# Kernel optimization log

Measured on AMD Instinct MI355X. Metric: run time of the kernel, lower is better.

## Reference

```python
import jax, jax.numpy as jnp
import numpy as np

N = 50000      # nodes
E = 800000     # edges (before self-loops)
FIN = 512      # in_channels
HID = 64       # hid_units[i]
HEADS = 8      # n_heads[i]
OUT = 40       # out_channels
NEG_SLOPE = 0.2


def setup_inputs() -> dict:
    key = jax.random.key(0)
    ks = jax.random.split(key, 16)
    d = {
        "x": jax.random.normal(ks[0], (N, FIN), dtype=jnp.float32),
        "edge_index": jax.random.randint(ks[1], (2, E), 0, N, dtype=jnp.int64),
        # layer 1: FIN -> HEADS*HID
        "W1": jax.random.normal(ks[2], (FIN, HEADS * HID), dtype=jnp.float32) * 0.05,
        "att_src1": jax.random.normal(ks[3], (HEADS, HID), dtype=jnp.float32) * 0.1,
        "att_dst1": jax.random.normal(ks[4], (HEADS, HID), dtype=jnp.float32) * 0.1,
        "b1": jnp.zeros((HEADS * HID,), dtype=jnp.float32),
        # layer 2: HEADS*HID -> HEADS*HID
        "W2": jax.random.normal(ks[5], (HEADS * HID, HEADS * HID), dtype=jnp.float32) * 0.05,
        "att_src2": jax.random.normal(ks[6], (HEADS, HID), dtype=jnp.float32) * 0.1,
        "att_dst2": jax.random.normal(ks[7], (HEADS, HID), dtype=jnp.float32) * 0.1,
        "b2": jnp.zeros((HEADS * HID,), dtype=jnp.float32),
        # output layer: HEADS*HID -> OUT, 1 head, concat=False
        "W3": jax.random.normal(ks[8], (HEADS * HID, OUT), dtype=jnp.float32) * 0.05,
        "att_src3": jax.random.normal(ks[9], (1, OUT), dtype=jnp.float32) * 0.1,
        "att_dst3": jax.random.normal(ks[10], (1, OUT), dtype=jnp.float32) * 0.1,
        "b3": jnp.zeros((OUT,), dtype=jnp.float32),
    }
    return d


def gat_conv(x, src, dst, W, a_src, a_dst, b, heads, out_ch, concat):
    # x: [N, Fin]; src/dst: [E'] (self-loops included)
    h = (x @ W).reshape(N, heads, out_ch)              # [N, H, C]
    alpha_src = jnp.sum(h * a_src[None], axis=-1)      # [N, H]
    alpha_dst = jnp.sum(h * a_dst[None], axis=-1)      # [N, H]
    e = jax.nn.leaky_relu(alpha_src[src] + alpha_dst[dst], NEG_SLOPE)  # [E', H]
    # segment softmax over edges grouped by target node
    m = jax.ops.segment_max(e, dst, num_segments=N)    # [N, H]
    ex = jnp.exp(e - m[dst])
    denom = jax.ops.segment_sum(ex, dst, num_segments=N)
    alpha = ex / denom[dst]                            # [E', H]
    out = jax.ops.segment_sum(h[src] * alpha[:, :, None], dst, num_segments=N)  # [N, H, C]
    out = out.reshape(N, heads * out_ch) if concat else out.mean(axis=1)
    return out + b


def reference(x, edge_index, W1, att_src1, att_dst1, b1,
              W2, att_src2, att_dst2, b2,
              W3, att_src3, att_dst3, b3):
    loop = jnp.arange(N, dtype=edge_index.dtype)
    src = jnp.concatenate([edge_index[0], loop])  # add_self_loops=True (PyG default)
    dst = jnp.concatenate([edge_index[1], loop])
    h = gat_conv(x, src, dst, W1, att_src1, att_dst1, b1, HEADS, HID, True)
    h = jax.nn.elu(h)  # dropout p=0.0 / eval -> identity
    h = gat_conv(h, src, dst, W2, att_src2, att_dst2, b2, HEADS, HID, True)
    h = jax.nn.elu(h)
    h = gat_conv(h, src, dst, W3, att_src3, att_dst3, b3, 1, OUT, False)
    return jax.nn.log_softmax(h, axis=1)
```

## Files before the change

kernel.cpp:

```cpp
#include <hip/hip_runtime.h>
#include <math.h>

#define NNODES 50000
#define NEDGES 800000
#define FINCH 512
#define HIDC 64
#define NHEADS 8
#define OUTC 40
#define NSLOPE 0.2f
#define NSB ((NNODES + 255) / 256)

typedef unsigned short ushort;
typedef unsigned int uint;
typedef unsigned char uchar;
typedef __attribute__((ext_vector_type(8))) short bf16x8;
typedef __attribute__((ext_vector_type(4))) float f32x4;
typedef __attribute__((ext_vector_type(2))) float f32x2;

#if __has_builtin(__builtin_amdgcn_cvt_pk_f32_fp8) && __has_builtin(__builtin_amdgcn_cvt_pk_fp8_f32)
#define HAS_FP8 1
#else
#define HAS_FP8 0
#endif

static __device__ __forceinline__ float leaky(float e) { return e > 0.f ? e : NSLOPE * e; }

static __device__ __forceinline__ float bf2f(ushort u) {
    union { unsigned int i; float f; } c; c.i = ((unsigned int)u) << 16; return c.f;
}
static __device__ __forceinline__ ushort f2bf(float f) {
    union { float f; unsigned int i; } c; c.f = f;
    unsigned int r = c.i + 0x7FFF + ((c.i >> 16) & 1);
    return (ushort)(r >> 16);
}
static __device__ __forceinline__ uint fkey(float f) {
    uint u = __float_as_uint(f);
    return (u & 0x80000000u) ? ~u : (u | 0x80000000u);
}
static __device__ __forceinline__ float fdec(uint k) {
    return __uint_as_float((k & 0x80000000u) ? (k & 0x7fffffffu) : ~k);
}

static __device__ __forceinline__ void gload16(const ushort* g, ushort* l) {
    __builtin_amdgcn_global_load_lds((const __attribute__((address_space(1))) void*)g,
                                     (__attribute__((address_space(3))) void*)l, 16, 0, 0);
}

__global__ __launch_bounds__(64) void k_detect(const int* __restrict__ ei, int* __restrict__ flag,
                                               uint* __restrict__ keys) {
    int lane = threadIdx.x;
    if (lane < 17) keys[lane] = fkey(-3.0e38f);
    int v = ei[2 * lane + 1];
    unsigned long long b = __ballot(v != 0);
    if (lane == 0) *flag = (b == 0ULL) ? 1 : 0;
}

static __device__ __forceinline__ int load_idx(const int* ei, int wide, int pos) {
    int v = wide ? ei[2 * (long long)pos] : ei[pos];
    v = v < 0 ? 0 : (v >= NNODES ? NNODES - 1 : v);
    return v;
}

__global__ void k_init_deg(int* __restrict__ deg) {
    int i = blockIdx.x * blockDim.x + threadIdx.x;
    if (i < NNODES) deg[i] = 1;
}

__global__ void k_count(const int* __restrict__ ei, const int* __restrict__ flag, int* __restrict__ deg) {
    int e = blockIdx.x * blockDim.x + threadIdx.x;
    if (e < NEDGES) {
        int d = load_idx(ei, *flag, NEDGES + e);
        atomicAdd(&deg[d], 1);
    }
}

__global__ __launch_bounds__(256) void k_bsum(const int* __restrict__ deg, int* __restrict__ bsum) {
    int i = blockIdx.x * 256 + threadIdx.x;
    int v = (i < NNODES) ? deg[i] : 0;
#pragma unroll
    for (int m = 32; m > 0; m >>= 1) v += __shfl_xor(v, m);
    __shared__ int ws[4];
    int wid = threadIdx.x >> 6, lane = threadIdx.x & 63;
    if (lane == 0) ws[wid] = v;
    __syncthreads();
    if (threadIdx.x == 0) bsum[blockIdx.x] = ws[0] + ws[1] + ws[2] + ws[3];
}

__global__ __launch_bounds__(64) void k_bscan(const int* __restrict__ bsum, int* __restrict__ bofs,
                                              int* __restrict__ offs) {
    const int lane = threadIdx.x;
    const int CH = (NSB + 63) / 64;
    int lo = lane * CH, hi = min(lo + CH, NSB);
    int s = 0;
    for (int i = lo; i < hi; i++) s += bsum[i];
    int x = s;
#pragma unroll
    for (int st = 1; st < 64; st <<= 1) { int v = __shfl_up(x, st); if (lane >= st) x += v; }
    int run = x - s;
    for (int i = lo; i < hi; i++) { bofs[i] = run; run += bsum[i]; }
    if (lane == 63) offs[NNODES] = run;
}

__global__ __launch_bounds__(256) void k_scan_final(const int* __restrict__ deg, const int* __restrict__ bofs,
                                                    int* __restrict__ offs, int* __restrict__ cur) {
    int b = blockIdx.x;
    int i = b * 256 + threadIdx.x;
    int v = (i < NNODES) ? deg[i] : 0;
    int lane = threadIdx.x & 63, wid = threadIdx.x >> 6;
    int x = v;
#pragma unroll
    for (int st = 1; st < 64; st <<= 1) { int t = __shfl_up(x, st); if (lane >= st) x += t; }
    __shared__ int ws[4];
    if (lane == 63) ws[wid] = x;
    __syncthreads();
    int wofs = 0;
#pragma unroll
    for (int w = 0; w < 4; w++) if (w < wid) wofs += ws[w];
    int excl = bofs[b] + wofs + x - v;
    if (i < NNODES) { offs[i] = excl; cur[i] = excl; }
}

__global__ void k_fill(const int* __restrict__ ei, const int* __restrict__ flag,
                       int* __restrict__ cur, int* __restrict__ csr) {
    int e = blockIdx.x * blockDim.x + threadIdx.x;
    if (e < NEDGES + NNODES) {
        int s, d;
        if (e < NEDGES) {
            int w = *flag;
            s = load_idx(ei, w, e);
            d = load_idx(ei, w, NEDGES + e);
        } else {
            s = e - NEDGES; d = s;
        }
        int pos = atomicAdd(&cur[d], 1);
        csr[pos] = s;
    }
}

template <int NH>
__global__ __launch_bounds__(256) void k_msrc(const float* __restrict__ src, uint* __restrict__ keys, int n) {
    float m = -3.0e38f;
    for (int i = blockIdx.x * 256 + threadIdx.x; i < n; i += gridDim.x * 256)
        m = fmaxf(m, src[i]);
    __shared__ float red[256];
    red[threadIdx.x] = m;
    __syncthreads();
    for (int st = 128; st >= NH; st >>= 1) {
        if (threadIdx.x < st) red[threadIdx.x] = fmaxf(red[threadIdx.x], red[threadIdx.x + st]);
        __syncthreads();
    }
    if (threadIdx.x < NH) atomicMax(&keys[threadIdx.x], fkey(red[threadIdx.x]));
}

__global__ void k_f2bf(const float* __restrict__ in, ushort* __restrict__ out, int n4) {
    int i = blockIdx.x * blockDim.x + threadIdx.x;
    if (i < n4) {
        float4 v = ((const float4*)in)[i];
        ushort4 o = make_ushort4(f2bf(v.x), f2bf(v.y), f2bf(v.z), f2bf(v.w));
        ((ushort4*)out)[i] = o;
    }
}

__global__ __launch_bounds__(256) void k_transpose(const float* __restrict__ W, ushort* __restrict__ Wt) {
    __shared__ float tile[32][33];
    int bx = blockIdx.x, by = blockIdx.y;
    int tx = threadIdx.x & 31, ty = threadIdx.x >> 5;
#pragma unroll
    for (int i = 0; i < 4; i++)
        tile[ty + i * 8][tx] = W[(size_t)(by * 32 + ty + i * 8) * 512 + bx * 32 + tx];
    __syncthreads();
#pragma unroll
    for (int i = 0; i < 4; i++)
        Wt[(size_t)(bx * 32 + ty + i * 8) * 512 + by * 32 + tx] = f2bf(tile[tx][ty + i * 8]);
}

__global__ __launch_bounds__(256) void k_transpose3(const float* __restrict__ W3, ushort* __restrict__ Wt3) {
    int idx = blockIdx.x * 256 + threadIdx.x;
    int c = idx >> 9, k = idx & 511;
    Wt3[idx] = (c < OUTC) ? f2bf(W3[(size_t)k * OUTC + c]) : 0;
}

template <int CMODE>
__global__ __launch_bounds__(512) void mfma_gemm2(const ushort* __restrict__ A, const ushort* __restrict__ Bt,
                                                  void* __restrict__ Cv,
                                                  const float* __restrict__ att_s, const float* __restrict__ att_d,
                                                  float* __restrict__ asrc, float* __restrict__ adst, int M) {
    __shared__ ushort Abuf[2][128 * 32];
    __shared__ ushort Bbuf[2][128 * 32];
    const int nwg = gridDim.x;
    const int q = nwg >> 3, r = nwg & 7;
    const int orig = blockIdx.x;
    const int xcd = orig & 7, ii = orig >> 3;
    const int wgid = (xcd < r ? xcd * (q + 1) : r * (q + 1) + (xcd - r) * q) + ii;
    const int row0 = (wgid >> 2) * 128, col0 = (wgid & 3) * 128;

    const int t = threadIdx.x;
    const int wid = t >> 6, lane = t & 63;
    const int wr = wid >> 1, wc = wid & 1;
    const int l15 = lane & 15, l4 = lane >> 4;
    const int arow = t >> 2, kb = t & 3;
    const int swz = (arow >> 1) & 3;
    const int ra = min(row0 + arow, M - 1);
    const ushort* gA = A + (size_t)ra * 512 + ((kb ^ swz) << 3);
    const ushort* gB = Bt + (size_t)(col0 + arow) * 512 + ((kb ^ swz) << 3);
    f32x4 acc[2][4] = {};

    gload16(gA, &Abuf[0][wid * 512]);
    gload16(gB, &Bbuf[0][wid * 512]);
    __syncthreads();
    int cur = 0;
    for (int k0 = 0; k0 < 512; k0 += 32) {
        if (k0 + 32 < 512) {
            gload16(gA + k0 + 32, &Abuf[cur ^ 1][wid * 512]);
            gload16(gB + k0 + 32, &Bbuf[cur ^ 1][wid * 512]);
        }
        bf16x8 af[2], bfr[4];
#pragma unroll
        for (int mr = 0; mr < 2; mr++) {
            int rr = wr * 32 + mr * 16 + l15;
            af[mr] = *(const bf16x8*)&Abuf[cur][rr * 32 + ((l4 ^ ((rr >> 1) & 3)) << 3)];
        }
#pragma unroll
        for (int nr = 0; nr < 4; nr++) {
            int cc = wc * 64 + nr * 16 + l15;
            bfr[nr] = *(const bf16x8*)&Bbuf[cur][cc * 32 + ((l4 ^ ((cc >> 1) & 3)) << 3)];
        }
#pragma unroll
        for (int mr = 0; mr < 2; mr++)
#pragma unroll
            for (int nr = 0; nr < 4; nr++)
                acc[mr][nr] = __builtin_amdgcn_mfma_f32_16x16x32_bf16(af[mr], bfr[nr], acc[mr][nr], 0, 0, 0);
        __syncthreads();
        cur ^= 1;
    }
#pragma unroll
    for (int mr = 0; mr < 2; mr++) {
#pragma unroll
        for (int qq = 0; qq < 4; qq++) {
            int gr = row0 + wr * 32 + mr * 16 + l4 * 4 + qq;
            if (gr >= M) continue;
#pragma unroll
            for (int nr = 0; nr < 4; nr++) {
                int gc = col0 + wc * 64 + nr * 16 + l15;
                if (CMODE == 0) {
                    ((ushort*)Cv)[(size_t)gr * 512 + gc] = f2bf(acc[mr][nr][qq]);
                } else {
#if HAS_FP8
                    uint pk = __builtin_amdgcn_cvt_pk_fp8_f32(acc[mr][nr][qq], acc[mr][nr][qq], 0, false);
                    ((uchar*)Cv)[(size_t)gr * 512 + gc] = (uchar)(pk & 0xff);
#endif
                }
            }
        }
    }
    const int hd = ((wgid & 3) << 1) | wc;
    float asf[4], adf[4];
#pragma unroll
    for (int nr = 0; nr < 4; nr++) {
        asf[nr] = att_s[hd * 64 + nr * 16 + l15];
        adf[nr] = att_d[hd * 64 + nr * 16 + l15];
    }
#pragma unroll
    for (int mr = 0; mr < 2; mr++) {
#pragma unroll
        for (int qq = 0; qq < 4; qq++) {
            float s1 = 0.f, s2 = 0.f;
#pragma unroll
            for (int nr = 0; nr < 4; nr++) {
                s1 = fmaf(acc[mr][nr][qq], asf[nr], s1);
                s2 = fmaf(acc[mr][nr][qq], adf[nr], s2);
            }
#pragma unroll
            for (int st = 1; st < 16; st <<= 1) {
                s1 += __shfl_xor(s1, st);
                s2 += __shfl_xor(s2, st);
            }
            int gr = row0 + wr * 32 + mr * 16 + l4 * 4 + qq;
            if (gr < M && l15 == 0) { asrc[gr * 8 + hd] = s1; adst[gr * 8 + hd] = s2; }
        }
    }
}

__global__ __launch_bounds__(256) void mfma_gemm3(const ushort* __restrict__ A, const ushort* __restrict__ Wt3,
                                                  float* __restrict__ h3, int M) {
    __shared__ ushort Abuf[2][64 * 32];
    __shared__ ushort Bbuf[2][64 * 32];
    const int t = threadIdx.x;
    const int wid = t >> 6, lane = t & 63;
    const int row0 = blockIdx.x * 64;
    const int l15 = lane & 15, l4 = lane >> 4;
    const int arow = t >> 2, kb = t & 3;
    const int swz = (arow >> 1) & 3;
    const int ra = min(row0 + arow, M - 1);
    const ushort* gA = A + (size_t)ra * 512 + ((kb ^ swz) << 3);
    const ushort* gB = Wt3 + (size_t)arow * 512 + ((kb ^ swz) << 3);
    f32x4 acc[4] = {};
    gload16(gA, &Abuf[0][wid * 512]);
    gload16(gB, &Bbuf[0][wid * 512]);
    __syncthreads();
    int cur = 0;
    for (int k0 = 0; k0 < 512; k0 += 32) {
        if (k0 + 32 < 512) {
            gload16(gA + k0 + 32, &Abuf[cur ^ 1][wid * 512]);
            gload16(gB + k0 + 32, &Bbuf[cur ^ 1][wid * 512]);
        }
        int rr = wid * 16 + l15;
        bf16x8 af = *(const bf16x8*)&Abuf[cur][rr * 32 + ((l4 ^ ((rr >> 1) & 3)) << 3)];
        bf16x8 bfr[4];
#pragma unroll
        for (int nr = 0; nr < 4; nr++) {
            int cc = nr * 16 + l15;
            bfr[nr] = *(const bf16x8*)&Bbuf[cur][cc * 32 + ((l4 ^ ((cc >> 1) & 3)) << 3)];
        }
#pragma unroll
        for (int nr = 0; nr < 4; nr++)
            acc[nr] = __builtin_amdgcn_mfma_f32_16x16x32_bf16(af, bfr[nr], acc[nr], 0, 0, 0);
        __syncthreads();
        cur ^= 1;
    }
#pragma unroll
    for (int qq = 0; qq < 4; qq++) {
        int gr = row0 + wid * 16 + l4 * 4 + qq;
        if (gr >= M) continue;
#pragma unroll
        for (int nr = 0; nr < 4; nr++) {
            int c = nr * 16 + l15;
            if (c < OUTC) h3[(size_t)gr * OUTC + c] = acc[nr][qq];
        }
    }
}

__global__ __launch_bounds__(256) void k_alpha1(const float* __restrict__ h, const float* __restrict__ att_s,
                                                const float* __restrict__ att_d, float* __restrict__ asrc,
                                                float* __restrict__ adst) {
    int gw = (blockIdx.x * 256 + threadIdx.x) >> 6;
    int lane = threadIdx.x & 63;
    if (gw >= NNODES) return;
    float s1 = 0.f, s2 = 0.f;
    if (lane < OUTC) {
        float v = h[(size_t)gw * OUTC + lane];
        s1 = v * att_s[lane];
        s2 = v * att_d[lane];
    }
#pragma unroll
    for (int m = 32; m > 0; m >>= 1) { s1 += __shfl_xor(s1, m); s2 += __shfl_xor(s2, m); }
    if (lane == 0) { asrc[gw] = s1; adst[gw] = s2; }
}

template <bool DO_ELU>
__global__ __launch_bounds__(256) void agg_v4(const ushort* __restrict__ h, const float* __restrict__ asrc,
                                              const float* __restrict__ adst, const int* __restrict__ offs,
                                              const int* __restrict__ csr, const float* __restrict__ bias,
                                              const uint* __restrict__ mkeys, ushort* __restrict__ out) {
    const int wid = threadIdx.x >> 6, lane = threadIdx.x & 63;
    const int n = blockIdx.x * 4 + wid;
    if (n >= NNODES) return;
    const int beg = offs[n], deg = offs[n + 1] - beg;
    const int h8 = lane & 7;
    const int es = lane >> 3;
    const float ad_s = adst[n * 8 + h8];
    const float m8 = leaky(fdec(mkeys[h8]) + ad_s);

    float ss = 0.f;
    for (int i = es; i < deg; i += 8) {
        int s = csr[beg + i];
        ss += expf(leaky(asrc[s * 8 + h8] + ad_s) - m8);
    }
    ss += __shfl_xor(ss, 8);
    ss += __shfl_xor(ss, 16);
    ss += __shfl_xor(ss, 32);
    const float rs8 = 1.f / ss;

    const int hc = lane >> 3;
    float acc[8] = {0.f, 0.f, 0.f, 0.f, 0.f, 0.f, 0.f, 0.f};
    int base = 0;
    for (; base + 8 <= deg; base += 8) {
        int sv = csr[beg + base + es];
        float wv = expf(leaky(asrc[sv * 8 + h8] + ad_s) - m8) * rs8;
#pragma unroll
        for (int j = 0; j < 8; j++) {
            int src = (j << 3) | hc;
            float w = __shfl(wv, src);
            int s = __shfl(sv, src);
            bf16x8 hv = *(const bf16x8*)(h + (size_t)s * FINCH + lane * 8);
#pragma unroll
            for (int c = 0; c < 8; c++) acc[c] = fmaf(bf2f((ushort)hv[c]), w, acc[c]);
        }
    }
    if (base < deg) {
        int e = base + es;
        int sv = csr[beg + min(e, deg - 1)];
        float wv = (e < deg) ? expf(leaky(asrc[sv * 8 + h8] + ad_s) - m8) * rs8 : 0.f;
        int cnt = deg - base;
        for (int j = 0; j < cnt; j++) {
            int src = (j << 3) | hc;
            float w = __shfl(wv, src);
            int s = __shfl(sv, src);
            bf16x8 hv = *(const bf16x8*)(h + (size_t)s * FINCH + lane * 8);
#pragma unroll
            for (int c = 0; c < 8; c++) acc[c] = fmaf(bf2f((ushort)hv[c]), w, acc[c]);
        }
    }
    ushort o[8];
#pragma unroll
    for (int c = 0; c < 8; c++) {
        float v = acc[c] + bias[lane * 8 + c];
        if (DO_ELU) v = v > 0.f ? v : expf(v) - 1.f;
        o[c] = f2bf(v);
    }
    *(bf16x8*)(out + (size_t)n * FINCH + lane * 8) = *(bf16x8*)o;
}

#if HAS_FP8
template <bool DO_ELU>
__global__ __launch_bounds__(256) void agg_v5(const uchar* __restrict__ h, const float* __restrict__ asrc,
                                              const float* __restrict__ adst, const int* __restrict__ offs,
                                              const int* __restrict__ csr, const float* __restrict__ bias,
                                              const uint* __restrict__ mkeys, ushort* __restrict__ out) {
    const int wid = threadIdx.x >> 6, lane = threadIdx.x & 63;
    const int n = blockIdx.x * 4 + wid;
    if (n >= NNODES) return;
    const int beg = offs[n], deg = offs[n + 1] - beg;
    const int h8 = lane & 7;
    const int es = lane >> 3;
    const float ad_s = adst[n * 8 + h8];
    const float m8 = leaky(fdec(mkeys[h8]) + ad_s);

    float ss = 0.f;
    for (int i = es; i < deg; i += 8) {
        int s = csr[beg + i];
        ss += expf(leaky(asrc[s * 8 + h8] + ad_s) - m8);
    }
    ss += __shfl_xor(ss, 8);
    ss += __shfl_xor(ss, 16);
    ss += __shfl_xor(ss, 32);
    const float rs8 = 1.f / ss;

    const int hc = lane >> 3;
    float acc[8] = {0.f, 0.f, 0.f, 0.f, 0.f, 0.f, 0.f, 0.f};
    int base = 0;
    for (; base + 8 <= deg; base += 8) {
        int sv = csr[beg + base + es];
        float wv = expf(leaky(asrc[sv * 8 + h8] + ad_s) - m8) * rs8;
#pragma unroll
        for (int j = 0; j < 8; j++) {
            int src = (j << 3) | hc;
            float w = __shfl(wv, src);
            int s = __shfl(sv, src);
            uint2 u = *(const uint2*)(h + (size_t)s * 512 + lane * 8);
            f32x2 p0 = __builtin_amdgcn_cvt_pk_f32_fp8(u.x, false);
            f32x2 p1 = __builtin_amdgcn_cvt_pk_f32_fp8(u.x, true);
            f32x2 p2 = __builtin_amdgcn_cvt_pk_f32_fp8(u.y, false);
            f32x2 p3 = __builtin_amdgcn_cvt_pk_f32_fp8(u.y, true);
            acc[0] = fmaf(p0[0], w, acc[0]); acc[1] = fmaf(p0[1], w, acc[1]);
            acc[2] = fmaf(p1[0], w, acc[2]); acc[3] = fmaf(p1[1], w, acc[3]);
            acc[4] = fmaf(p2[0], w, acc[4]); acc[5] = fmaf(p2[1], w, acc[5]);
            acc[6] = fmaf(p3[0], w, acc[6]); acc[7] = fmaf(p3[1], w, acc[7]);
        }
    }
    if (base < deg) {
        int e = base + es;
        int sv = csr[beg + min(e, deg - 1)];
        float wv = (e < deg) ? expf(leaky(asrc[sv * 8 + h8] + ad_s) - m8) * rs8 : 0.f;
        int cnt = deg - base;
        for (int j = 0; j < cnt; j++) {
            int src = (j << 3) | hc;
            float w = __shfl(wv, src);
            int s = __shfl(sv, src);
            uint2 u = *(const uint2*)(h + (size_t)s * 512 + lane * 8);
            f32x2 p0 = __builtin_amdgcn_cvt_pk_f32_fp8(u.x, false);
            f32x2 p1 = __builtin_amdgcn_cvt_pk_f32_fp8(u.x, true);
            f32x2 p2 = __builtin_amdgcn_cvt_pk_f32_fp8(u.y, false);
            f32x2 p3 = __builtin_amdgcn_cvt_pk_f32_fp8(u.y, true);
            acc[0] = fmaf(p0[0], w, acc[0]); acc[1] = fmaf(p0[1], w, acc[1]);
            acc[2] = fmaf(p1[0], w, acc[2]); acc[3] = fmaf(p1[1], w, acc[3]);
            acc[4] = fmaf(p2[0], w, acc[4]); acc[5] = fmaf(p2[1], w, acc[5]);
            acc[6] = fmaf(p3[0], w, acc[6]); acc[7] = fmaf(p3[1], w, acc[7]);
        }
    }
    ushort o[8];
#pragma unroll
    for (int c = 0; c < 8; c++) {
        float v = acc[c] + bias[lane * 8 + c];
        if (DO_ELU) v = v > 0.f ? v : expf(v) - 1.f;
        o[c] = f2bf(v);
    }
    *(bf16x8*)(out + (size_t)n * FINCH + lane * 8) = *(bf16x8*)o;
}
#endif

__global__ __launch_bounds__(64) void agg_out(const float* __restrict__ h3, const float* __restrict__ asrc,
                                              const float* __restrict__ adst, const int* __restrict__ offs,
                                              const int* __restrict__ csr, const float* __restrict__ bias,
                                              const uint* __restrict__ mkeys, float* __restrict__ out) {
    const int n = blockIdx.x, lane = threadIdx.x;
    const int beg = offs[n], deg = offs[n + 1] - beg;
    const float ad = adst[n];
    const float m = leaky(fdec(mkeys[0]) + ad);

    float ss = 0.f;
    for (int i = lane; i < deg; i += 64) ss += expf(leaky(asrc[csr[beg + i]] + ad) - m);
#pragma unroll
    for (int w = 32; w > 0; w >>= 1) ss += __shfl_xor(ss, w);
    float rs = 1.f / ss;

    float acc = 0.f;
    for (int base = 0; base < deg; base += 64) {
        int sv = (base + lane < deg) ? csr[beg + base + lane] : 0;
        int cnt = min(64, deg - base);
        int j = 0;
        for (; j + 2 <= cnt; j += 2) {
            int s0 = __shfl(sv, j), s1 = __shfl(sv, j + 1);
            float a0 = asrc[s0], a1 = asrc[s1];
            float v0 = (lane < OUTC) ? h3[(size_t)s0 * OUTC + lane] : 0.f;
            float v1 = (lane < OUTC) ? h3[(size_t)s1 * OUTC + lane] : 0.f;
            float w0 = expf(leaky(a0 + ad) - m) * rs;
            float w1 = expf(leaky(a1 + ad) - m) * rs;
            acc = fmaf(v0, w0, acc);
            acc = fmaf(v1, w1, acc);
        }
        if (j < cnt) {
            int s0 = __shfl(sv, j);
            float w0 = expf(leaky(asrc[s0] + ad) - m) * rs;
            float v0 = (lane < OUTC) ? h3[(size_t)s0 * OUTC + lane] : 0.f;
            acc = fmaf(v0, w0, acc);
        }
    }
    float v = (lane < OUTC) ? acc + bias[lane] : -1e30f;
    float mx = v;
#pragma unroll
    for (int w = 32; w > 0; w >>= 1) mx = fmaxf(mx, __shfl_xor(mx, w));
    float ex = (lane < OUTC) ? expf(v - mx) : 0.f;
    float se = ex;
#pragma unroll
    for (int w = 32; w > 0; w >>= 1) se += __shfl_xor(se, w);
    if (lane < OUTC) out[(size_t)n * OUTC + lane] = v - mx - logf(se);
}

extern "C" void kernel_launch(void* const* d_in, const int* in_sizes, int n_in,
                              void* d_out, int out_size, void* d_ws, size_t ws_size,
                              hipStream_t stream) {
    const float* x   = (const float*)d_in[0];
    const int*   ei  = (const int*)d_in[1];
    const float* W1  = (const float*)d_in[2];
    const float* as1 = (const float*)d_in[3];
    const float* ad1 = (const float*)d_in[4];
    const float* b1  = (const float*)d_in[5];
    const float* W2  = (const float*)d_in[6];
    const float* as2 = (const float*)d_in[7];
    const float* ad2 = (const float*)d_in[8];
    const float* b2  = (const float*)d_in[9];
    const float* W3  = (const float*)d_in[10];
    const float* as3 = (const float*)d_in[11];
    const float* ad3 = (const float*)d_in[12];
    const float* b3  = (const float*)d_in[13];
    float* out = (float*)d_out;

    char* p = (char*)d_ws;
    ushort* bufA = (ushort*)p; p += (size_t)NNODES * FINCH * 2;
    ushort* bufB = (ushort*)p; p += (size_t)NNODES * FINCH * 2;
    float* asrc = (float*)p; p += (size_t)NNODES * 8 * 4;
    float* adst = (float*)p; p += (size_t)NNODES * 8 * 4;
    int* flag = (int*)p; p += 16;
    uint* mkeys = (uint*)p; p += 128;
    int* deg  = (int*)p; p += (size_t)NNODES * 4;
    int* offs = (int*)p; p += (size_t)(NNODES + 1) * 4;
    int* cur  = (int*)p; p += (size_t)NNODES * 4;
    int* csr  = (int*)p; p += (size_t)(NEDGES + NNODES) * 4;
    ushort* Wt1 = (ushort*)p; p += (size_t)512 * 512 * 2;
    ushort* Wt2 = (ushort*)p; p += (size_t)512 * 512 * 2;
    ushort* Wt3 = (ushort*)p; p += (size_t)64 * 512 * 2;
    int* bsum = (int*)p; p += (size_t)NSB * 4;
    int* bofs = (int*)p; p += (size_t)NSB * 4;
    float* h3 = (float*)bufA;
    float* asc3 = asrc;
    float* adc3 = adst;

    k_detect<<<1, 64, 0, stream>>>(ei, flag, mkeys);
    k_init_deg<<<(NNODES + 255) / 256, 256, 0, stream>>>(deg);
    k_count<<<(NEDGES + 255) / 256, 256, 0, stream>>>(ei, flag, deg);
    k_bsum<<<NSB, 256, 0, stream>>>(deg, bsum);
    k_bscan<<<1, 64, 0, stream>>>(bsum, bofs, offs);
    k_scan_final<<<NSB, 256, 0, stream>>>(deg, bofs, offs, cur);
    k_fill<<<(NEDGES + NNODES + 255) / 256, 256, 0, stream>>>(ei, flag, cur, csr);

    {
        int n4 = NNODES * FINCH / 4;
        k_f2bf<<<(n4 + 255) / 256, 256, 0, stream>>>(x, bufB, n4);
        dim3 gt(16, 16);
        k_transpose<<<gt, 256, 0, stream>>>(W1, Wt1);
        k_transpose<<<gt, 256, 0, stream>>>(W2, Wt2);
        k_transpose3<<<128, 256, 0, stream>>>(W3, Wt3);
    }

    int nwg = 4 * ((NNODES + 127) / 128);
    int gagg = (NNODES + 3) / 4;
#if HAS_FP8
    mfma_gemm2<1><<<nwg, 512, 0, stream>>>(bufB, Wt1, bufA, as1, ad1, asrc, adst, NNODES);
    k_msrc<8><<<128, 256, 0, stream>>>(asrc, mkeys, NNODES * 8);
    agg_v5<true><<<gagg, 256, 0, stream>>>((const uchar*)bufA, asrc, adst, offs, csr, b1, mkeys, bufB);
#else
    mfma_gemm2<0><<<nwg, 512, 0, stream>>>(bufB, Wt1, bufA, as1, ad1, asrc, adst, NNODES);
    k_msrc<8><<<128, 256, 0, stream>>>(asrc, mkeys, NNODES * 8);
    agg_v4<true><<<gagg, 256, 0, stream>>>(bufA, asrc, adst, offs, csr, b1, mkeys, bufB);
#endif
    mfma_gemm2<0><<<nwg, 512, 0, stream>>>(bufB, Wt2, bufA, as2, ad2, asrc, adst, NNODES);
    k_msrc<8><<<128, 256, 0, stream>>>(asrc, mkeys + 8, NNODES * 8);
    agg_v4<true><<<gagg, 256, 0, stream>>>(bufA, asrc, adst, offs, csr, b2, mkeys + 8, bufB);
    mfma_gemm3<<<(NNODES + 63) / 64, 256, 0, stream>>>(bufB, Wt3, h3, NNODES);
    k_alpha1<<<(NNODES * 64 + 255) / 256, 256, 0, stream>>>(h3, as3, ad3, asc3, adc3);
    k_msrc<1><<<128, 256, 0, stream>>>(asc3, mkeys + 16, NNODES);
    agg_out<<<NNODES, 64, 0, stream>>>(h3, asc3, adc3, offs, csr, b3, mkeys + 16, out);
}
```

Before: 597.2 us.

## Restructure GEMM to keep full-K B slice in LDS, stream A from global

The 512-K GEMM used for layers 1 and 2 is restructured. Each workgroup now computes a 128x64 tile, one head, and preloads the full 64x512 B slice into swizzled LDS once. A fragments are read directly from global memory instead of going through the double-buffered K loop with per-step barriers. Per-row attention dots are combined across the two wave columns through LDS before writing. This doubles the grid and the number of reads of A, and relies on cache hits to avoid extra traffic. It also simplifies the XCD remapping, which now assumes nwg is divisible by 8.

```diff
diff --git a/kernel.cpp b/kernel.cpp
--- a/kernel.cpp
+++ b/kernel.cpp
@@ -185,54 +185,47 @@
                                                   void* __restrict__ Cv,
                                                   const float* __restrict__ att_s, const float* __restrict__ att_d,
                                                   float* __restrict__ asrc, float* __restrict__ adst, int M) {
-    __shared__ ushort Abuf[2][128 * 32];
-    __shared__ ushort Bbuf[2][128 * 32];
+    __shared__ ushort Blds[64 * 512];
     const int nwg = gridDim.x;
-    const int q = nwg >> 3, r = nwg & 7;
     const int orig = blockIdx.x;
-    const int xcd = orig & 7, ii = orig >> 3;
-    const int wgid = (xcd < r ? xcd * (q + 1) : r * (q + 1) + (xcd - r) * q) + ii;
-    const int row0 = (wgid >> 2) * 128, col0 = (wgid & 3) * 128;
+    const int wgid = (orig & 7) * (nwg >> 3) + (orig >> 3);
+    const int row0 = (wgid >> 3) * 128;
+    const int cb = wgid & 7;
+    const int col0 = cb * 64;
 
     const int t = threadIdx.x;
     const int wid = t >> 6, lane = t & 63;
     const int wr = wid >> 1, wc = wid & 1;
     const int l15 = lane & 15, l4 = lane >> 4;
-    const int arow = t >> 2, kb = t & 3;
-    const int swz = (arow >> 1) & 3;
-    const int ra = min(row0 + arow, M - 1);
-    const ushort* gA = A + (size_t)ra * 512 + ((kb ^ swz) << 3);
-    const ushort* gB = Bt + (size_t)(col0 + arow) * 512 + ((kb ^ swz) << 3);
-    f32x4 acc[2][4] = {};
-
-    gload16(gA, &Abuf[0][wid * 512]);
-    gload16(gB, &Bbuf[0][wid * 512]);
-    __syncthreads();
-    int cur = 0;
-    for (int k0 = 0; k0 < 512; k0 += 32) {
-        if (k0 + 32 < 512) {
-            gload16(gA + k0 + 32, &Abuf[cur ^ 1][wid * 512]);
-            gload16(gB + k0 + 32, &Bbuf[cur ^ 1][wid * 512]);
-        }
-        bf16x8 af[2], bfr[4];
-#pragma unroll
-        for (int mr = 0; mr < 2; mr++) {
-            int rr = wr * 32 + mr * 16 + l15;
-            af[mr] = *(const bf16x8*)&Abuf[cur][rr * 32 + ((l4 ^ ((rr >> 1) & 3)) << 3)];
-        }
-#pragma unroll
-        for (int nr = 0; nr < 4; nr++) {
-            int cc = wc * 64 + nr * 16 + l15;
-            bfr[nr] = *(const bf16x8*)&Bbuf[cur][cc * 32 + ((l4 ^ ((cc >> 1) & 3)) << 3)];
-        }
-#pragma unroll
-        for (int mr = 0; mr < 2; mr++)
-#pragma unroll
-            for (int nr = 0; nr < 4; nr++)
-                acc[mr][nr] = __builtin_amdgcn_mfma_f32_16x16x32_bf16(af[mr], bfr[nr], acc[mr][nr], 0, 0, 0);
-        __syncthreads();
-        cur ^= 1;
-    }
+
+#pragma unroll
+    for (int it = 0; it < 8; it++) {
+        int rr = wid * 8 + it;
+        const ushort* src = Bt + (size_t)(col0 + rr) * 512 + (((lane * 16) ^ ((rr & 7) << 4)) >> 1);
+        gload16(src, &Blds[rr * 512]);
+    }
+    __syncthreads();
+
+    f32x4 acc[2][2] = {};
+    const int r0 = row0 + wr * 32 + l15;
+    const ushort* gA0 = A + (size_t)min(r0, M - 1) * 512 + l4 * 8;
+    const ushort* gA1 = A + (size_t)min(r0 + 16, M - 1) * 512 + l4 * 8;
+
+#pragma unroll
+    for (int k = 0; k < 16; k++) {
+        bf16x8 a0 = *(const bf16x8*)(gA0 + k * 32);
+        bf16x8 a1 = *(const bf16x8*)(gA1 + k * 32);
+        int c0 = wc * 32 + l15;
+        int c1 = c0 + 16;
+        int off = k * 64 + l4 * 16;
+        bf16x8 b0 = *(const bf16x8*)((const char*)Blds + c0 * 1024 + (off ^ ((c0 & 7) << 4)));
+        bf16x8 b1 = *(const bf16x8*)((const char*)Blds + c1 * 1024 + (off ^ ((c1 & 7) << 4)));
+        acc[0][0] = __builtin_amdgcn_mfma_f32_16x16x32_bf16(a0, b0, acc[0][0], 0, 0, 0);
+        acc[0][1] = __builtin_amdgcn_mfma_f32_16x16x32_bf16(a0, b1, acc[0][1], 0, 0, 0);
+        acc[1][0] = __builtin_amdgcn_mfma_f32_16x16x32_bf16(a1, b0, acc[1][0], 0, 0, 0);
+        acc[1][1] = __builtin_amdgcn_mfma_f32_16x16x32_bf16(a1, b1, acc[1][1], 0, 0, 0);
+    }
+
 #pragma unroll
     for (int mr = 0; mr < 2; mr++) {
 #pragma unroll
@@ -240,8 +233,8 @@
             int gr = row0 + wr * 32 + mr * 16 + l4 * 4 + qq;
             if (gr >= M) continue;
 #pragma unroll
-            for (int nr = 0; nr < 4; nr++) {
-                int gc = col0 + wc * 64 + nr * 16 + l15;
+            for (int nr = 0; nr < 2; nr++) {
+                int gc = col0 + wc * 32 + nr * 16 + l15;
                 if (CMODE == 0) {
                     ((ushort*)Cv)[(size_t)gr * 512 + gc] = f2bf(acc[mr][nr][qq]);
                 } else {
@@ -253,20 +246,22 @@
             }
         }
     }
-    const int hd = ((wgid & 3) << 1) | wc;
-    float asf[4], adf[4];
-#pragma unroll
-    for (int nr = 0; nr < 4; nr++) {
-        asf[nr] = att_s[hd * 64 + nr * 16 + l15];
-        adf[nr] = att_d[hd * 64 + nr * 16 + l15];
-    }
+
+    float asf[2], adf[2];
+#pragma unroll
+    for (int nr = 0; nr < 2; nr++) {
+        int gc = wc * 32 + nr * 16 + l15;
+        asf[nr] = att_s[cb * 64 + gc];
+        adf[nr] = att_d[cb * 64 + gc];
+    }
+    float p1[2][4], p2[2][4];
 #pragma unroll
     for (int mr = 0; mr < 2; mr++) {
 #pragma unroll
         for (int qq = 0; qq < 4; qq++) {
             float s1 = 0.f, s2 = 0.f;
 #pragma unroll
-            for (int nr = 0; nr < 4; nr++) {
+            for (int nr = 0; nr < 2; nr++) {
                 s1 = fmaf(acc[mr][nr][qq], asf[nr], s1);
                 s2 = fmaf(acc[mr][nr][qq], adf[nr], s2);
             }
@@ -275,8 +270,27 @@
                 s1 += __shfl_xor(s1, st);
                 s2 += __shfl_xor(s2, st);
             }
-            int gr = row0 + wr * 32 + mr * 16 + l4 * 4 + qq;
-            if (gr < M && l15 == 0) { asrc[gr * 8 + hd] = s1; adst[gr * 8 + hd] = s2; }
+            p1[mr][qq] = s1; p2[mr][qq] = s2;
+        }
+    }
+    __syncthreads();
+    float* aP = (float*)Blds;
+    if (l15 == 0) {
+#pragma unroll
+        for (int mr = 0; mr < 2; mr++)
+#pragma unroll
+            for (int qq = 0; qq < 4; qq++) {
+                int lr = wr * 32 + mr * 16 + l4 * 4 + qq;
+                aP[lr * 2 + wc] = p1[mr][qq];
+                aP[256 + lr * 2 + wc] = p2[mr][qq];
+            }
+    }
+    __syncthreads();
+    if (t < 128) {
+        int gr = row0 + t;
+        if (gr < M) {
+            asrc[gr * 8 + cb] = aP[t * 2] + aP[t * 2 + 1];
+            adst[gr * 8 + cb] = aP[256 + t * 2] + aP[256 + t * 2 + 1];
         }
     }
 }
@@ -593,7 +607,7 @@
         k_transpose3<<<128, 256, 0, stream>>>(W3, Wt3);
     }
 
-    int nwg = 4 * ((NNODES + 127) / 128);
+    int nwg = 8 * ((NNODES + 127) / 128);
     int gagg = (NNODES + 3) / 4;
 #if HAS_FP8
     mfma_gemm2<1><<<nwg, 512, 0, stream>>>(bufB, Wt1, bufA, as1, ad1, asrc, adst, NNODES);
```

Result: slower. 718.4 us (+20.3%).
